# Kernel tuning notes

Measured on AMD Instinct MI355X. Metric: run time of the kernel, lower is better.

The kernel has to match this reference:

```python
import jax, jax.numpy as jnp
import numpy as np

B, N, D_IN, D_OUT = 16, 2048, 128, 128

def setup_inputs() -> dict:
    key = jax.random.key(0)
    ks = jax.random.split(key, 8)
    x = jax.random.normal(ks[0], (B, N, D_IN), dtype=jnp.float32)
    adj = jax.random.randint(ks[1], (N, N), 0, 2).astype(jnp.float32)
    # Conv1d(kernel_size=1) weights, PyTorch default uniform init scale
    s_emb = 1.0 / np.sqrt(D_IN)
    W_emb = jax.random.uniform(ks[2], (D_OUT, D_IN), jnp.float32, -s_emb, s_emb)
    b_emb = jax.random.uniform(ks[3], (D_OUT,), jnp.float32, -s_emb, s_emb)
    s_qk = 1.0 / np.sqrt(D_OUT)
    w_q = jax.random.uniform(ks[4], (D_OUT,), jnp.float32, -s_qk, s_qk)
    b_q = jax.random.uniform(ks[5], (1,), jnp.float32, -s_qk, s_qk)
    w_k = jax.random.uniform(ks[6], (D_OUT,), jnp.float32, -s_qk, s_qk)
    b_k = jax.random.uniform(ks[7], (1,), jnp.float32, -s_qk, s_qk)
    return {"x": x, "adj": adj, "W_emb": W_emb, "b_emb": b_emb,
            "w_q": w_q, "b_q": b_q, "w_k": w_k, "b_k": b_k}

def reference(x, adj, W_emb, b_emb, w_q, b_q, w_k, b_k):
    # emb_conv: 1x1 conv over node dim == per-node linear  [B,N,D_out]
    seq_fts = jnp.einsum('bni,oi->bno', x, W_emb) + b_emb
    # q_conv / k_conv: project to scalar per node  [B,N]
    q = jnp.einsum('bnd,d->bn', seq_fts, w_q) + b_q  # f_1_t squeezed
    k = jnp.einsum('bnd,d->bn', seq_fts, w_k) + b_k  # f_2_t squeezed
    # f[b,i,j] = f_1_t[b,0,j] + f_2_t^T[b,i,0] = q[b,j] + k[b,i]
    f = k[:, :, None] + q[:, None, :]                 # [B,N,N]
    f = jax.nn.leaky_relu(adj[None, :, :] * f, negative_slope=0.01)
    coefs = jax.nn.softmax(f, axis=1)                 # softmax over dim=1 (rows)
    vals = jnp.einsum('bij,bjd->bid', coefs, seq_fts)  # [B,N,D_out]
    return vals
```

## Files before the change

### kernel.cpp

```cpp
#include <hip/hip_runtime.h>
#include <hip/hip_bf16.h>
#include <stdint.h>

#define B_ 16
#define N_ 2048
#define D_ 128

typedef __bf16 bf16_t;
typedef bf16_t bf16x8 __attribute__((ext_vector_type(8)));
typedef float f32x4 __attribute__((ext_vector_type(4)));

__global__ __launch_bounds__(256) void k_pack_adj(const float* __restrict__ adj,
                                                  unsigned int* __restrict__ bits) {
    int t = blockIdx.x * 256 + threadIdx.x;
    float v = adj[t];
    unsigned long long m = __ballot(v > 0.5f);
    if ((t & 63) == 0) {
        int i = t >> 11;
        int j = t & 2047;
        bits[i * 64 + (j >> 5)]     = (unsigned int)m;
        bits[i * 64 + (j >> 5) + 1] = (unsigned int)(m >> 32);
    }
}

__global__ __launch_bounds__(256, 2) void k_emb(const float* __restrict__ x,
                                                const float* __restrict__ W,
                                                const float* __restrict__ be,
                                                const float* __restrict__ wq,
                                                const float* __restrict__ bq,
                                                const float* __restrict__ wk,
                                                const float* __restrict__ bk,
                                                bf16_t* __restrict__ Pb,
                                                float* __restrict__ qa, float* __restrict__ ka,
                                                float* __restrict__ Eq, float* __restrict__ eqs,
                                                float* __restrict__ Ek, float* __restrict__ eks,
                                                float* __restrict__ denom) {
    __shared__ float xs[32][68];
    __shared__ float ws[32][132];
    __shared__ float qs[64], ks[64];
    int b  = blockIdx.y;
    int n0 = blockIdx.x * 64;
    int tid = threadIdx.x;
    int tx = tid & 15, ty = tid >> 4;
    if (tid < 64) { qs[tid] = 0.f; ks[tid] = 0.f; }

    float acc[4][8] = {};
    f32x4 xr[2], wr[4];

    auto loadregs = [&](int kc) {
#pragma unroll
        for (int s = 0; s < 2; ++s) {
            int p = tid + 256 * s;
            int n = p >> 3, kq = p & 7;
            xr[s] = *(const f32x4*)(x + ((size_t)(b * N_ + n0 + n)) * D_ + kc * 32 + kq * 4);
        }
#pragma unroll
        for (int s = 0; s < 4; ++s) {
            int p = tid + 256 * s;
            int d = p >> 3, kq = p & 7;
            wr[s] = *(const f32x4*)(W + (size_t)d * D_ + kc * 32 + kq * 4);
        }
    };
    auto writelds = [&]() {
#pragma unroll
        for (int s = 0; s < 2; ++s) {
            int p = tid + 256 * s;
            int n = p >> 3, kq = p & 7;
#pragma unroll
            for (int u = 0; u < 4; ++u) xs[kq * 4 + u][n] = xr[s][u];
        }
#pragma unroll
        for (int s = 0; s < 4; ++s) {
            int p = tid + 256 * s;
            int d = p >> 3, kq = p & 7;
#pragma unroll
            for (int u = 0; u < 4; ++u) ws[kq * 4 + u][d] = wr[s][u];
        }
    };

    loadregs(0);
    for (int kc = 0; kc < 4; ++kc) {
        writelds();
        __syncthreads();
        if (kc < 3) loadregs(kc + 1);
#pragma unroll 4
        for (int k = 0; k < 32; ++k) {
            f32x4 xv  = *(const f32x4*)&xs[k][tx * 4];
            f32x4 wv0 = *(const f32x4*)&ws[k][ty * 8];
            f32x4 wv1 = *(const f32x4*)&ws[k][ty * 8 + 4];
#pragma unroll
            for (int i = 0; i < 4; ++i)
#pragma unroll
                for (int j = 0; j < 8; ++j)
                    acc[i][j] += xv[i] * ((j < 4) ? wv0[j] : wv1[j - 4]);
        }
        __syncthreads();
    }

    float qp[4] = {}, kp[4] = {};
#pragma unroll
    for (int j = 0; j < 8; ++j) {
        int d = ty * 8 + j;
        float bj  = be[d];
        float wqj = wq[d];
        float wkj = wk[d];
        f32x4 o;
        bf16_t ob[4];
#pragma unroll
        for (int i = 0; i < 4; ++i) {
            o[i] = acc[i][j] + bj;
            qp[i] += o[i] * wqj;
            kp[i] += o[i] * wkj;
            ob[i] = (bf16_t)o[i];
        }
        *(uint2*)(Pb + ((size_t)b * D_ + d) * N_ + n0 + tx * 4) = *(uint2*)ob;
    }
#pragma unroll
    for (int i = 0; i < 4; ++i) {
        atomicAdd(&qs[tx * 4 + i], qp[i]);
        atomicAdd(&ks[tx * 4 + i], kp[i]);
    }
    __syncthreads();
    if (tid < 64) {
        int idx = b * N_ + n0 + tid;
        float aq = qs[tid] + bq[0];
        float ak = ks[tid] + bk[0];
        qa[idx] = aq;          ka[idx] = ak;
        Eq[idx] = expf(aq);    eqs[idx] = expf(0.01f * aq);
        Ek[idx] = expf(ak);    eks[idx] = expf(0.01f * ak);
        denom[idx] = 0.f;
    }
}

__global__ __launch_bounds__(256) void k_denom(const unsigned int* __restrict__ bits,
                                               const float* __restrict__ qa,
                                               const float* __restrict__ ka,
                                               const float* __restrict__ Eq,
                                               const float* __restrict__ eqs,
                                               const float* __restrict__ Ek,
                                               const float* __restrict__ eks,
                                               float* __restrict__ denom) {
    int jt  = blockIdx.x;
    int b   = blockIdx.y;
    int seg = blockIdx.z;
    int j = jt * 256 + threadIdx.x;
    float qj  = qa[b * N_ + j];
    float Eqj = Eq[b * N_ + j];
    float eqj = eqs[b * N_ + j];
    int shift = j & 31;
    int wid   = j >> 5;
    float acc = 0.f;
    int i0 = seg * 256;
#pragma unroll 16
    for (int i = i0; i < i0 + 256; ++i) {
        float kk  = ka[b * N_ + i];
        float Ekk = Ek[b * N_ + i];
        float ekk = eks[b * N_ + i];
        unsigned int w = bits[i * 64 + wid];
        float z  = kk + qj;
        float f1 = z > 0.f ? Ekk : ekk;
        float f2 = z > 0.f ? Eqj : eqj;
        float v  = f1 * f2;
        acc += ((w >> shift) & 1u) ? v : 1.0f;
    }
    atomicAdd(&denom[b * N_ + j], acc);
}

__global__ __launch_bounds__(256) void k_post(const float* __restrict__ denom,
                                              const float* __restrict__ Eq,
                                              const float* __restrict__ eqs,
                                              float* __restrict__ rd,
                                              float* __restrict__ Eqr,
                                              float* __restrict__ eqr) {
    int t = blockIdx.x * 256 + threadIdx.x;
    float r = 1.0f / denom[t];
    rd[t]  = r;
    Eqr[t] = Eq[t] * r;
    eqr[t] = eqs[t] * r;
}

__global__ __launch_bounds__(256, 2) void k_attn(const float* __restrict__ qa,
                                                 const float* __restrict__ ka,
                                                 const float* __restrict__ Ek,
                                                 const float* __restrict__ eks,
                                                 const float* __restrict__ rd,
                                                 const float* __restrict__ Eqr,
                                                 const float* __restrict__ eqr,
                                                 const unsigned int* __restrict__ bits,
                                                 const bf16_t* __restrict__ Pb,
                                                 float* __restrict__ out) {
    __shared__ __align__(16) bf16_t ldsB[2][128 * 64];
    __shared__ __align__(16) bf16_t ldsA[4 * 2 * 64 * 8];
    int b     = blockIdx.y;
    int ibase = blockIdx.x * 64;
    int tid   = threadIdx.x;
    int w     = tid >> 6;
    int lane  = tid & 63;
    int m16   = lane & 15;
    int quad  = lane >> 4;
    int ig    = w & 1;
    int dg    = w >> 1;

    int iA = ibase + (2 * ig) * 16 + m16;
    int iB = iA + 16;
    float mkR0 = -ka[b * N_ + iA], mkR1 = -ka[b * N_ + iB];
    float EkR0 = Ek[b * N_ + iA],  EkR1 = Ek[b * N_ + iB];
    float ekR0 = eks[b * N_ + iA], ekR1 = eks[b * N_ + iB];
    const unsigned int* brA = bits + (size_t)iA * 64;
    const unsigned int* brB = bits + (size_t)iB * 64;
    const float* qp  = qa  + b * N_;
    const float* Erp = Eqr + b * N_;
    const float* erp = eqr + b * N_;
    const float* rdp = rd  + b * N_;
    const bf16_t* PtB = Pb + (size_t)b * D_ * N_;

    f32x4 acc[2][4];
#pragma unroll
    for (int c = 0; c < 2; ++c)
#pragma unroll
        for (int nt = 0; nt < 4; ++nt) acc[c][nt] = (f32x4){0.f, 0.f, 0.f, 0.f};

    f32x4 qv4[2][2], Er4[2][2], er4[2][2], rd4[2][2];
    unsigned int mA[2], mB[2];

    auto ldj = [&](int par, int jb) {
        int j0 = jb + dg * 32 + quad * 8;
        qv4[par][0] = *(const f32x4*)(qp  + j0);
        qv4[par][1] = *(const f32x4*)(qp  + j0 + 4);
        Er4[par][0] = *(const f32x4*)(Erp + j0);
        Er4[par][1] = *(const f32x4*)(Erp + j0 + 4);
        er4[par][0] = *(const f32x4*)(erp + j0);
        er4[par][1] = *(const f32x4*)(erp + j0 + 4);
        rd4[par][0] = *(const f32x4*)(rdp + j0);
        rd4[par][1] = *(const f32x4*)(rdp + j0 + 4);
        mA[par] = brA[(jb >> 5) + dg];
        mB[par] = brB[(jb >> 5) + dg];
    };

    auto stage = [&](int bufi, int jb) {
#pragma unroll
        for (int t = 0; t < 4; ++t) {
            int off = t * 4096 + tid * 16;
            int d   = off >> 7;
            int g   = ((off & 127) >> 4) ^ (d & 7);
            const bf16_t* gp = PtB + (size_t)d * N_ + jb + g * 8;
            __builtin_amdgcn_global_load_lds(
                (const __attribute__((address_space(1))) void*)gp,
                (__attribute__((address_space(3))) void*)((char*)(&ldsB[bufi][0]) + off),
                16, 0, 0);
        }
    };

    auto agen = [&](int par, bf16x8& afA, bf16x8& afB) {
#pragma unroll
        for (int t = 0; t < 8; ++t) {
            float qv = (t < 4) ? qv4[par][0][t] : qv4[par][1][t - 4];
            float Er = (t < 4) ? Er4[par][0][t] : Er4[par][1][t - 4];
            float er = (t < 4) ? er4[par][0][t] : er4[par][1][t - 4];
            float rj = (t < 4) ? rd4[par][0][t] : rd4[par][1][t - 4];
            int bit = quad * 8 + t;
            {
                bool c = qv > mkR0;
                float v = (c ? EkR0 : ekR0) * (c ? Er : er);
                afA[t] = (bf16_t)(((mA[par] >> bit) & 1u) ? v : rj);
            }
            {
                bool c = qv > mkR1;
                float v = (c ? EkR1 : ekR1) * (c ? Er : er);
                afB[t] = (bf16_t)(((mB[par] >> bit) & 1u) ? v : rj);
            }
        }
        *(bf16x8*)((char*)ldsA + ((((2 * ig + 0) * 2 + dg) * 64 + lane) * 16)) = afA;
        *(bf16x8*)((char*)ldsA + ((((2 * ig + 1) * 2 + dg) * 64 + lane) * 16)) = afB;
    };

    auto mfma_phase = [&](int buf, const bf16x8& afA, const bf16x8& afB) {
        {
            int cph = ((dg * 4 + quad) ^ (m16 & 7)) * 8;
#pragma unroll
            for (int nt = 0; nt < 4; ++nt) {
                int d = dg * 64 + nt * 16 + m16;
                bf16x8 bf = *(const bf16x8*)&ldsB[buf][d * 64 + cph];
                acc[0][nt] = __builtin_amdgcn_mfma_f32_16x16x32_bf16(afA, bf, acc[0][nt], 0, 0, 0);
                acc[1][nt] = __builtin_amdgcn_mfma_f32_16x16x32_bf16(afB, bf, acc[1][nt], 0, 0, 0);
            }
        }
        {
            int oh = 1 - dg;
            bf16x8 a0 = *(const bf16x8*)((char*)ldsA + ((((2 * ig + 0) * 2 + oh) * 64 + lane) * 16));
            bf16x8 a1 = *(const bf16x8*)((char*)ldsA + ((((2 * ig + 1) * 2 + oh) * 64 + lane) * 16));
            int cph = ((oh * 4 + quad) ^ (m16 & 7)) * 8;
#pragma unroll
            for (int nt = 0; nt < 4; ++nt) {
                int d = dg * 64 + nt * 16 + m16;
                bf16x8 bf = *(const bf16x8*)&ldsB[buf][d * 64 + cph];
                acc[0][nt] = __builtin_amdgcn_mfma_f32_16x16x32_bf16(a0, bf, acc[0][nt], 0, 0, 0);
                acc[1][nt] = __builtin_amdgcn_mfma_f32_16x16x32_bf16(a1, bf, acc[1][nt], 0, 0, 0);
            }
        }
    };

    stage(0, 0);
    ldj(0, 0);
    int buf = 0;
#pragma unroll 1
    for (int s2 = 0; s2 < 15; ++s2) {
#pragma unroll
        for (int par = 0; par < 2; ++par) {
            int jb = (s2 * 2 + par) * 64;
            ldj(par ^ 1, jb + 64);
            stage(buf ^ 1, jb + 64);

            bf16x8 afA, afB;
            agen(par, afA, afB);
            asm volatile("s_waitcnt vmcnt(14) lgkmcnt(0)" ::: "memory");
            __builtin_amdgcn_s_barrier();

            mfma_phase(buf, afA, afB);

            asm volatile("s_waitcnt lgkmcnt(0)" ::: "memory");
            __builtin_amdgcn_s_barrier();
            buf ^= 1;
        }
    }
    {
        ldj(1, 31 * 64);
        stage(buf ^ 1, 31 * 64);
        bf16x8 afA, afB;
        agen(0, afA, afB);
        asm volatile("s_waitcnt vmcnt(14) lgkmcnt(0)" ::: "memory");
        __builtin_amdgcn_s_barrier();
        mfma_phase(buf, afA, afB);
        asm volatile("s_waitcnt lgkmcnt(0)" ::: "memory");
        __builtin_amdgcn_s_barrier();
        buf ^= 1;
    }
    {
        bf16x8 afA, afB;
        agen(1, afA, afB);
        asm volatile("s_waitcnt vmcnt(0) lgkmcnt(0)" ::: "memory");
        __builtin_amdgcn_s_barrier();
        mfma_phase(buf, afA, afB);
    }

#pragma unroll
    for (int c = 0; c < 2; ++c) {
        int irow = ibase + (2 * ig + c) * 16 + quad * 4;
#pragma unroll
        for (int nt = 0; nt < 4; ++nt) {
            int d = dg * 64 + nt * 16 + m16;
#pragma unroll
            for (int r = 0; r < 4; ++r)
                out[((size_t)b * N_ + irow + r) * D_ + d] = acc[c][nt][r];
        }
    }
}

extern "C" void kernel_launch(void* const* d_in, const int* in_sizes, int n_in,
                              void* d_out, int out_size, void* d_ws, size_t ws_size,
                              hipStream_t stream) {
    const float* x   = (const float*)d_in[0];
    const float* adj = (const float*)d_in[1];
    const float* W   = (const float*)d_in[2];
    const float* be  = (const float*)d_in[3];
    const float* wq  = (const float*)d_in[4];
    const float* bq  = (const float*)d_in[5];
    const float* wk  = (const float*)d_in[6];
    const float* bk  = (const float*)d_in[7];
    float* out = (float*)d_out;

    char* ws = (char*)d_ws;
    size_t off = 0;
    bf16_t* Pb = (bf16_t*)(ws + off); off += (size_t)B_ * D_ * N_ * 2;
    float* qa  = (float*)(ws + off);  off += (size_t)B_ * N_ * 4;
    float* ka  = (float*)(ws + off);  off += (size_t)B_ * N_ * 4;
    float* denom = (float*)(ws + off); off += (size_t)B_ * N_ * 4;
    float* Eq  = (float*)(ws + off);  off += (size_t)B_ * N_ * 4;
    float* eqs = (float*)(ws + off);  off += (size_t)B_ * N_ * 4;
    float* Ek  = (float*)(ws + off);  off += (size_t)B_ * N_ * 4;
    float* eks = (float*)(ws + off);  off += (size_t)B_ * N_ * 4;
    float* rd  = (float*)(ws + off);  off += (size_t)B_ * N_ * 4;
    float* Eqr = (float*)(ws + off);  off += (size_t)B_ * N_ * 4;
    float* eqr = (float*)(ws + off);  off += (size_t)B_ * N_ * 4;
    unsigned int* bits = (unsigned int*)(ws + off); off += (size_t)N_ * 64 * 4;

    k_pack_adj<<<N_ * N_ / 256, 256, 0, stream>>>(adj, bits);
    k_emb<<<dim3(N_ / 64, B_), 256, 0, stream>>>(x, W, be, wq, bq, wk, bk,
                                                 Pb, qa, ka, Eq, eqs, Ek, eks, denom);
    k_denom<<<dim3(8, 16, 8), 256, 0, stream>>>(bits, qa, ka, Eq, eqs, Ek, eks, denom);
    k_post<<<B_ * N_ / 256, 256, 0, stream>>>(denom, Eq, eqs, rd, Eqr, eqr);
    k_attn<<<dim3(N_ / 64, B_), 256, 0, stream>>>(qa, ka, Ek, eks, rd, Eqr, eqr,
                                                  bits, Pb, out);
}
```

Baseline: 186.3 us.

## Split attention reduction over j into two halves with atomic output accumulation

The attention kernel's j-loop is split across a new grid z-dimension of 2, so each block handles half the columns and accumulates its partial result into the output with float atomics. The output is zeroed in the post kernel, and launch bounds are raised to 4 blocks per CU. This doubles the grid (512 to 1024 blocks) to improve CU occupancy and tail balance. The cost is atomic traffic on the full output tensor, an extra zeroing pass, and possible register pressure from the higher occupancy target.

```diff
diff --git a/kernel.cpp b/kernel.cpp
--- a/kernel.cpp
+++ b/kernel.cpp
@@ -171,15 +171,21 @@
                                               const float* __restrict__ eqs,
                                               float* __restrict__ rd,
                                               float* __restrict__ Eqr,
-                                              float* __restrict__ eqr) {
+                                              float* __restrict__ eqr,
+                                              float* __restrict__ out) {
     int t = blockIdx.x * 256 + threadIdx.x;
     float r = 1.0f / denom[t];
     rd[t]  = r;
     Eqr[t] = Eq[t] * r;
     eqr[t] = eqs[t] * r;
-}
-
-__global__ __launch_bounds__(256, 2) void k_attn(const float* __restrict__ qa,
+    f32x4* o4 = (f32x4*)out;
+#pragma unroll
+    for (int z = 0; z < (B_ * N_ * D_ / 4) / (B_ * N_); ++z)
+        o4[t + z * (B_ * N_)] = (f32x4){0.f, 0.f, 0.f, 0.f};
+}
+
+#define JSTEPS_ (N_ / 2 / 64)
+__global__ __launch_bounds__(256, 4) void k_attn(const float* __restrict__ qa,
                                                  const float* __restrict__ ka,
                                                  const float* __restrict__ Ek,
                                                  const float* __restrict__ eks,
@@ -193,6 +199,7 @@
     __shared__ __align__(16) bf16_t ldsA[4 * 2 * 64 * 8];
     int b     = blockIdx.y;
     int ibase = blockIdx.x * 64;
+    int j0    = blockIdx.z * (N_ / 2);
     int tid   = threadIdx.x;
     int w     = tid >> 6;
     int lane  = tid & 63;
@@ -224,15 +231,15 @@
     unsigned int mA[2], mB[2];
 
     auto ldj = [&](int par, int jb) {
-        int j0 = jb + dg * 32 + quad * 8;
-        qv4[par][0] = *(const f32x4*)(qp  + j0);
-        qv4[par][1] = *(const f32x4*)(qp  + j0 + 4);
-        Er4[par][0] = *(const f32x4*)(Erp + j0);
-        Er4[par][1] = *(const f32x4*)(Erp + j0 + 4);
-        er4[par][0] = *(const f32x4*)(erp + j0);
-        er4[par][1] = *(const f32x4*)(erp + j0 + 4);
-        rd4[par][0] = *(const f32x4*)(rdp + j0);
-        rd4[par][1] = *(const f32x4*)(rdp + j0 + 4);
+        int j0l = jb + dg * 32 + quad * 8;
+        qv4[par][0] = *(const f32x4*)(qp  + j0l);
+        qv4[par][1] = *(const f32x4*)(qp  + j0l + 4);
+        Er4[par][0] = *(const f32x4*)(Erp + j0l);
+        Er4[par][1] = *(const f32x4*)(Erp + j0l + 4);
+        er4[par][0] = *(const f32x4*)(erp + j0l);
+        er4[par][1] = *(const f32x4*)(erp + j0l + 4);
+        rd4[par][0] = *(const f32x4*)(rdp + j0l);
+        rd4[par][1] = *(const f32x4*)(rdp + j0l + 4);
         mA[par] = brA[(jb >> 5) + dg];
         mB[par] = brB[(jb >> 5) + dg];
     };
@@ -300,14 +307,14 @@
         }
     };
 
-    stage(0, 0);
-    ldj(0, 0);
+    stage(0, j0);
+    ldj(0, j0);
     int buf = 0;
 #pragma unroll 1
-    for (int s2 = 0; s2 < 15; ++s2) {
+    for (int s2 = 0; s2 < JSTEPS_ / 2 - 1; ++s2) {
 #pragma unroll
         for (int par = 0; par < 2; ++par) {
-            int jb = (s2 * 2 + par) * 64;
+            int jb = j0 + (s2 * 2 + par) * 64;
             ldj(par ^ 1, jb + 64);
             stage(buf ^ 1, jb + 64);
 
@@ -324,8 +331,9 @@
         }
     }
     {
-        ldj(1, 31 * 64);
-        stage(buf ^ 1, 31 * 64);
+        int jb = j0 + (JSTEPS_ - 2) * 64;
+        ldj(1, jb + 64);
+        stage(buf ^ 1, jb + 64);
         bf16x8 afA, afB;
         agen(0, afA, afB);
         asm volatile("s_waitcnt vmcnt(14) lgkmcnt(0)" ::: "memory");
@@ -351,7 +359,7 @@
             int d = dg * 64 + nt * 16 + m16;
 #pragma unroll
             for (int r = 0; r < 4; ++r)
-                out[((size_t)b * N_ + irow + r) * D_ + d] = acc[c][nt][r];
+                atomicAdd(&out[((size_t)b * N_ + irow + r) * D_ + d], acc[c][nt][r]);
         }
     }
 }
@@ -388,7 +396,7 @@
     k_emb<<<dim3(N_ / 64, B_), 256, 0, stream>>>(x, W, be, wq, bq, wk, bk,
                                                  Pb, qa, ka, Eq, eqs, Ek, eks, denom);
     k_denom<<<dim3(8, 16, 8), 256, 0, stream>>>(bits, qa, ka, Eq, eqs, Ek, eks, denom);
-    k_post<<<B_ * N_ / 256, 256, 0, stream>>>(denom, Eq, eqs, rd, Eqr, eqr);
-    k_attn<<<dim3(N_ / 64, B_), 256, 0, stream>>>(qa, ka, Ek, eks, rd, Eqr, eqr,
-                                                  bits, Pb, out);
-}
+    k_post<<<B_ * N_ / 256, 256, 0, stream>>>(denom, Eq, eqs, rd, Eqr, eqr, out);
+    k_attn<<<dim3(N_ / 64, B_, 2), 256, 0, stream>>>(qa, ka, Ek, eks, rd, Eqr, eqr,
+                                                     bits, Pb, out);
+}
```

Measured after the change: 268.9 us. 1.44x slower.
